# Performance work log

Measured on AMD Instinct MI355X. Metric: run time of the kernel, lower is better.

## Reference

```python
import math
import jax, jax.numpy as jnp
import numpy as np

B, N, D = 16, 4096, 256
N_CAT, N_TPC, N_VPT, N_SP = 16, 8, 4, 16
N_TYPE = N_CAT * N_TPC          # 128
N_VAR = N_TYPE * N_VPT          # 512
THRESH = 0.1
MASK_VAL = jnp.finfo(jnp.float32).min / 2


def _linear(x, w, b):
    # torch nn.Linear: y = x @ W^T + b, W: (out, in)
    return x @ w.T + b


def _level(codes, proj_w, proj_b, K, X, mask, tau):
    """One codebook level: attention of codes over tokens.
    codes: (M, d). Returns H:(B,M,d), w_raw:(B,M)."""
    Q = _linear(codes, proj_w, proj_b)                       # (M, d)
    attn = jnp.einsum('md,bnd->bmn', Q, K) / math.sqrt(D)    # (B, M, N)
    attn = jnp.where(mask[:, None, :], attn, MASK_VAL)
    attn = jnp.clip(attn, -50.0, 50.0)
    G = jnp.nan_to_num(jax.nn.softmax(attn, axis=-1))        # (B, M, N)
    H = jnp.einsum('bmn,bnd->bmd', G, X)                     # (B, M, d)
    w_raw = jnp.linalg.norm(H, axis=-1) / tau                # (B, M)
    return H, w_raw


def _sparsify(w, thr):
    ws = jnp.where(w > thr, w, 0.0)
    return ws / (ws.sum(axis=-1, keepdims=True) + 1e-8)


def _forward(X, positions, category_codes, type_codes, variant_codes,
             spatial_codes, log_tau, cat_w, cat_b, type_w, type_b,
             var_w, var_b, sp_w, sp_b, k_w, k_b, g1_w, g1_b, g2_w, g2_b,
             out_w, out_b, ln_g, ln_b, level_weights, mask):
    tau = jnp.clip(jnp.exp(log_tau[0]) + 0.1, 0.1, 2.0)
    K = _linear(X, k_w, k_b)                                 # (B, N, d)

    # Level 0: category
    H_cat, w_cat_raw = _level(category_codes, cat_w, cat_b, K, X, mask, tau)
    w_cat = jax.nn.softmax(w_cat_raw, axis=-1)
    w_cat_sp = _sparsify(w_cat, THRESH)

    # Level 1: type, gated by category selection
    H_type, w_type_raw = _level(type_codes.reshape(-1, D), type_w, type_b,
                                K, X, mask, tau)
    w_t = (w_type_raw.reshape(-1, N_CAT, N_TPC) * w_cat_sp[:, :, None]
           ).reshape(-1, N_TYPE)
    w_type = jax.nn.softmax(w_t, axis=-1)
    w_type_sp = _sparsify(w_type, THRESH / 2)

    # Level 2: variant, gated by type selection
    H_var, w_var_raw = _level(variant_codes.reshape(-1, D), var_w, var_b,
                              K, X, mask, tau)
    w_type_exp = jnp.repeat(w_type_sp, N_VPT, axis=-1)       # (B, 512)
    w_var = jax.nn.softmax(w_var_raw * w_type_exp, axis=-1)
    w_var_sp = _sparsify(w_var, THRESH / 4)

    # Spatial level (independent)
    H_sp, w_sp_raw = _level(spatial_codes, sp_w, sp_b, K, X, mask, tau)
    w_sp = jax.nn.softmax(w_sp_raw, axis=-1)
    w_sp_sp = _sparsify(w_sp, THRESH)

    z_cat = jnp.einsum('bm,bmd->bd', w_cat_sp, H_cat)
    z_type = jnp.einsum('bm,bmd->bd', w_type_sp, H_type)
    z_var = jnp.einsum('bm,bmd->bd', w_var_sp, H_var)
    z_spatial = jnp.einsum('bm,bmd->bd', w_sp_sp, H_sp)

    # Position gating of category summary
    mask_f = mask.astype(X.dtype)[:, :, None]
    pos_pooled = (positions * mask_f).sum(1) / jnp.maximum(mask_f.sum(1), 1.0)
    gate_in = jnp.concatenate([z_cat, pos_pooled], axis=-1)  # (B, 2d)
    h = jax.nn.gelu(_linear(gate_in, g1_w, g1_b), approximate=False)
    pos_gate = jax.nn.sigmoid(_linear(h, g2_w, g2_b))
    z_cat = z_cat * pos_gate

    # Learned level combine + gated output projection
    lw = jax.nn.softmax(level_weights)
    z = (lw[0] * z_cat + lw[1] * z_type + lw[2] * z_var + lw[3] * z_spatial)
    z = _linear(z, out_w, out_b)
    mu = z.mean(-1, keepdims=True)
    var = z.var(-1, keepdims=True)
    z = (z - mu) / jnp.sqrt(var + 1e-5) * ln_g + ln_b
    return z


def setup_inputs() -> dict:
    key = jax.random.key(0)
    ks = jax.random.split(key, 32)
    s = 1.0 / math.sqrt(D)
    inp = {
        'X': jax.random.normal(ks[0], (B, N, D), jnp.float32),
        'positions': jax.random.normal(ks[1], (B, N, D), jnp.float32),
        'category_codes': jax.random.normal(ks[2], (N_CAT, D)) * 0.02,
        'type_codes': jax.random.normal(ks[3], (N_CAT, N_TPC, D)) * 0.02,
        'variant_codes': jax.random.normal(ks[4], (N_CAT, N_TPC, N_VPT, D)) * 0.02,
        'spatial_codes': jax.random.normal(ks[5], (N_SP, D)) * 0.02,
        'log_tau': jnp.zeros((1,), jnp.float32),
        'cat_w': jax.random.normal(ks[6], (D, D)) * s,
        'cat_b': jnp.zeros((D,)),
        'type_w': jax.random.normal(ks[7], (D, D)) * s,
        'type_b': jnp.zeros((D,)),
        'var_w': jax.random.normal(ks[8], (D, D)) * s,
        'var_b': jnp.zeros((D,)),
        'sp_w': jax.random.normal(ks[9], (D, D)) * s,
        'sp_b': jnp.zeros((D,)),
        'k_w': jax.random.normal(ks[10], (D, D)) * s,
        'k_b': jnp.zeros((D,)),
        'g1_w': jax.random.normal(ks[11], (D, 2 * D)) * s,
        'g1_b': jnp.zeros((D,)),
        'g2_w': jax.random.normal(ks[12], (D, D)) * s,
        'g2_b': jnp.zeros((D,)),
        'out_w': jax.random.normal(ks[13], (D, D)) * s,
        'out_b': jnp.zeros((D,)),
        'ln_g': jnp.ones((D,)),
        'ln_b': jnp.zeros((D,)),
        'level_weights': jnp.ones((4,)) / 4.0,
        'mask': jnp.ones((B, N), jnp.bool_),
    }
    return inp


def reference(X, positions, category_codes, type_codes, variant_codes,
              spatial_codes, log_tau, cat_w, cat_b, type_w, type_b,
              var_w, var_b, sp_w, sp_b, k_w, k_b, g1_w, g1_b, g2_w, g2_b,
              out_w, out_b, ln_g, ln_b, level_weights, mask):
    return _forward(X, positions, category_codes, type_codes, variant_codes,
                    spatial_codes, log_tau, cat_w, cat_b, type_w, type_b,
                    var_w, var_b, sp_w, sp_b, k_w, k_b, g1_w, g1_b,
                    g2_w, g2_b, out_w, out_b, ln_g, ln_b, level_weights, mask)
```

## Files before the change

kernel.cpp:

```cpp
#include <hip/hip_runtime.h>


#define DEV static __device__ __forceinline__

typedef short bf16x8 __attribute__((ext_vector_type(8)));
typedef float f32x4 __attribute__((ext_vector_type(4)));
typedef unsigned short u16x8 __attribute__((ext_vector_type(8)));

DEV float bf2f(unsigned short u) {
  return __uint_as_float(((unsigned int)u) << 16);
}
DEV unsigned short f2bf(float f) {
  unsigned int x = __float_as_uint(f);
  unsigned int r = (x + 0x7fffu + ((x >> 16) & 1u)) >> 16;
  return (unsigned short)r;
}

DEV void gl2lds16(const void* g, void* l) {
  __builtin_amdgcn_global_load_lds(
      (const __attribute__((address_space(1))) unsigned int*)g,
      (__attribute__((address_space(3))) unsigned int*)l, 16, 0, 0);
}

DEV bf16x8 pack8(const float4 a, const float4 b) {
  bf16x8 r;
  r[0] = (short)f2bf(a.x); r[1] = (short)f2bf(a.y);
  r[2] = (short)f2bf(a.z); r[3] = (short)f2bf(a.w);
  r[4] = (short)f2bf(b.x); r[5] = (short)f2bf(b.y);
  r[6] = (short)f2bf(b.z); r[7] = (short)f2bf(b.w);
  return r;
}

DEV size_t pk_off(int rt, int ks) { return ((size_t)rt * 8 + ks) * 512; }

__global__ __launch_bounds__(256) void kproj_mfma(
    const float* __restrict__ X, const float* __restrict__ W,
    const float* __restrict__ bias, unsigned short* __restrict__ Kp) {
  __shared__ __align__(16) unsigned short As[128 * 72];
  __shared__ __align__(16) unsigned short Bs[128 * 72];
  const int m0 = blockIdx.x * 128, c0 = blockIdx.y * 128;
  const int t = threadIdx.x, l = t & 63, w = t >> 6;
  const int wm = (w & 1) * 64, wn = (w >> 1) * 64;
  const f32x4 zero = {0.f, 0.f, 0.f, 0.f};
  f32x4 acc[4][4];
#pragma unroll
  for (int i = 0; i < 4; ++i)
#pragma unroll
    for (int j = 0; j < 4; ++j) acc[i][j] = zero;
  const int rr = t >> 3, cc = (t & 7) * 8;
  for (int kc = 0; kc < 256; kc += 64) {
    __syncthreads();
#pragma unroll
    for (int p = 0; p < 4; ++p) {
      const int r = p * 32 + rr;
      const float* xs = &X[(size_t)(m0 + r) * 256 + kc + cc];
      const float4 a0 = *(const float4*)&xs[0];
      const float4 a1 = *(const float4*)&xs[4];
      *(bf16x8*)&As[r * 72 + cc] = pack8(a0, a1);
      const float* wsrc = &W[(size_t)(c0 + r) * 256 + kc + cc];
      const float4 b0 = *(const float4*)&wsrc[0];
      const float4 b1 = *(const float4*)&wsrc[4];
      *(bf16x8*)&Bs[r * 72 + cc] = pack8(b0, b1);
    }
    __syncthreads();
#pragma unroll
    for (int ks = 0; ks < 2; ++ks) {
      const int koff = ks * 32 + ((l >> 4) & 3) * 8;
      bf16x8 a[4], b[4];
#pragma unroll
      for (int f = 0; f < 4; ++f)
        a[f] = *(const bf16x8*)&As[(wm + f * 16 + (l & 15)) * 72 + koff];
#pragma unroll
      for (int f = 0; f < 4; ++f)
        b[f] = *(const bf16x8*)&Bs[(wn + f * 16 + (l & 15)) * 72 + koff];
#pragma unroll
      for (int i = 0; i < 4; ++i)
#pragma unroll
        for (int j = 0; j < 4; ++j)
          acc[i][j] =
              __builtin_amdgcn_mfma_f32_16x16x32_bf16(a[i], b[j], acc[i][j],
                                                      0, 0, 0);
    }
  }
  const int q = (l >> 4) & 3;
#pragma unroll
  for (int j = 0; j < 4; ++j) {
    const int c = c0 + wn + j * 16 + (l & 15);
    const float bv = bias[c];
#pragma unroll
    for (int i = 0; i < 4; ++i) {
      const int mrow = m0 + wm + i * 16 + q * 4;
#pragma unroll
      for (int r = 0; r < 4; ++r) {
        const int m = mrow + r;
        Kp[pk_off(m >> 4, c >> 5) + ((m & 15) + 16 * ((c >> 3) & 3)) * 8 +
           (c & 7)] = f2bf(acc[i][j][r] + bv);
      }
    }
  }
}

__global__ __launch_bounds__(256) void xT_kern(const float* __restrict__ X,
                                               unsigned short* __restrict__ XTp) {
  __shared__ float Ls[64][65];
  const int tn = blockIdx.x, td = blockIdx.y, b = blockIdx.z;
  const int t = threadIdx.x;
  const int nl = t >> 2, dp = (t & 3) * 16;
  const float* src =
      X + ((size_t)b * 4096 + tn * 64 + nl) * 256 + td * 64 + dp;
#pragma unroll
  for (int v = 0; v < 4; ++v) {
    const float4 x = *(const float4*)&src[v * 4];
    Ls[nl][dp + v * 4 + 0] = x.x;
    Ls[nl][dp + v * 4 + 1] = x.y;
    Ls[nl][dp + v * 4 + 2] = x.z;
    Ls[nl][dp + v * 4 + 3] = x.w;
  }
  __syncthreads();
  const int dl = t >> 2, np = (t & 3) * 16;
  u16x8 h0, h1;
#pragma unroll
  for (int j = 0; j < 8; ++j) h0[j] = f2bf(Ls[np + j][dl]);
#pragma unroll
  for (int j = 0; j < 8; ++j) h1[j] = f2bf(Ls[np + 8 + j][dl]);
  const int d = td * 64 + dl;
  const int n0g = tn * 64 + np;
  const int n1g = n0g + 8;
  unsigned short* dst = XTp + (size_t)b * 1048576;
  const size_t o0 = (((size_t)(d >> 4) * 128) + (n0g >> 5)) * 512 +
                    ((d & 15) + 16 * ((n0g >> 3) & 3)) * 8;
  const size_t o1 = (((size_t)(d >> 4) * 128) + (n1g >> 5)) * 512 +
                    ((d & 15) + 16 * ((n1g >> 3) & 3)) * 8;
  *(u16x8*)&dst[o0] = h0;
  *(u16x8*)&dst[o1] = h1;
}

__global__ __launch_bounds__(256) void qproj_kern(
    const float* __restrict__ cat_codes, const float* __restrict__ type_codes,
    const float* __restrict__ var_codes, const float* __restrict__ sp_codes,
    const float* __restrict__ cat_w, const float* __restrict__ cat_b,
    const float* __restrict__ type_w, const float* __restrict__ type_b,
    const float* __restrict__ var_w, const float* __restrict__ var_b,
    const float* __restrict__ sp_w, const float* __restrict__ sp_b,
    unsigned short* __restrict__ Qp) {
  const int m = blockIdx.x;
  const int t = threadIdx.x;
  const size_t off = pk_off(m >> 4, t >> 5) +
                     ((m & 15) + 16 * ((t >> 3) & 3)) * 8 + (t & 7);
  if (m >= 672) {
    Qp[off] = 0;
    return;
  }
  const float* code;
  const float* W;
  const float* bias;
  if (m < 16)       { code = cat_codes  + m * 256;         W = cat_w;  bias = cat_b; }
  else if (m < 144) { code = type_codes + (m - 16) * 256;  W = type_w; bias = type_b; }
  else if (m < 656) { code = var_codes  + (m - 144) * 256; W = var_w;  bias = var_b; }
  else              { code = sp_codes   + (m - 656) * 256; W = sp_w;   bias = sp_b; }
  __shared__ float xs[256];
  xs[t] = code[t];
  __syncthreads();
  float a = bias[t];
  const float* wr = W + (size_t)t * 256;
  for (int k = 0; k < 256; k += 4) {
    const float4 w = *(const float4*)&wr[k];
    a = fmaf(w.x, xs[k], a);
    a = fmaf(w.y, xs[k + 1], a);
    a = fmaf(w.z, xs[k + 2], a);
    a = fmaf(w.w, xs[k + 3], a);
  }
  Qp[off] = f2bf(a);
}

__global__ __launch_bounds__(256, 3) void attn_fused(
    const unsigned short* __restrict__ Qp, const unsigned short* __restrict__ Kp,
    const unsigned short* __restrict__ XTp,
    const unsigned char* __restrict__ mask, float* __restrict__ H,
    float* __restrict__ lsum) {
  __shared__ __align__(16) unsigned short Ks[16384];
  __shared__ __align__(16) unsigned short Plds[64 * 72];
  __shared__ unsigned char msk[1024];
  const int combo = blockIdx.x;
  const int m0 = blockIdx.y * 64;
  const int b = combo >> 2;
  const int nbase = (combo & 3) * 1024;
  const int t = threadIdx.x, l = t & 63, w = t >> 6;
  const int l15 = l & 15, q = l >> 4;
  ((uchar4*)msk)[t] = ((const uchar4*)(mask + (size_t)b * 4096 + nbase))[t];
  const int mt_g = (m0 >> 4) + w;
  bf16x8 qf[8];
#pragma unroll
  for (int ks = 0; ks < 8; ++ks)
    qf[ks] = *(const bf16x8*)&Qp[pk_off(mt_g, ks) + l * 8];
  const f32x4 zero = {0.f, 0.f, 0.f, 0.f};
  f32x4 accO[4][4];
#pragma unroll
  for (int i = 0; i < 4; ++i)
#pragma unroll
    for (int j = 0; j < 4; ++j) accO[i][j] = zero;
  f32x4 rs = zero;
  const unsigned short* XTb = XTp + (size_t)b * 1048576;
  const unsigned short* Kchunk0 = Kp + ((size_t)b * 256 + (nbase >> 4)) * 4096;
#pragma unroll
  for (int i = 0; i < 8; ++i)
    gl2lds16(Kchunk0 + (w * 8 + i) * 512 + l * 8, &Ks[(w * 8 + i) * 512]);
  for (int c = 0; c < 16; ++c) {
    __syncthreads();
    const int nst0 = (nbase >> 5) + c * 2;
    bf16x8 xf[2][4];
#pragma unroll
    for (int ks2 = 0; ks2 < 2; ++ks2)
#pragma unroll
      for (int dj = 0; dj < 4; ++dj)
        xf[ks2][dj] = *(const bf16x8*)&XTb[((size_t)(4 * w + dj) * 128 +
                                            nst0 + ks2) * 512 + l * 8];
    f32x4 accS[4];
#pragma unroll
    for (int f = 0; f < 4; ++f) accS[f] = zero;
    __builtin_amdgcn_s_setprio(1);
#pragma unroll
    for (int ks = 0; ks < 8; ++ks) {
      bf16x8 kf[4];
#pragma unroll
      for (int f = 0; f < 4; ++f)
        kf[f] = *(const bf16x8*)&Ks[(f * 8 + ks) * 512 + l * 8];
#pragma unroll
      for (int f = 0; f < 4; ++f)
        accS[f] = __builtin_amdgcn_mfma_f32_16x16x32_bf16(qf[ks], kf[f],
                                                          accS[f], 0, 0, 0);
    }
    __builtin_amdgcn_s_setprio(0);
#pragma unroll
    for (int f = 0; f < 4; ++f) {
      const bool mk = msk[c * 64 + f * 16 + l15] != 0;
#pragma unroll
      for (int r = 0; r < 4; ++r) {
        float s = accS[f][r] * 0.0625f;
        s = fminf(fmaxf(s, -50.f), 50.f);
        if (!mk) s = -50.f;
        const float e = __expf(s);
        Plds[(w * 16 + q * 4 + r) * 72 + f * 16 + l15] = f2bf(e);
        rs[r] += e;
      }
    }
    __syncthreads();
    if (c < 15) {
      const unsigned short* src = Kchunk0 + (size_t)(c + 1) * 16384;
#pragma unroll
      for (int i = 0; i < 8; ++i)
        gl2lds16(src + (w * 8 + i) * 512 + l * 8, &Ks[(w * 8 + i) * 512]);
    }
#pragma unroll
    for (int ks2 = 0; ks2 < 2; ++ks2) {
      bf16x8 pf[4];
#pragma unroll
      for (int mt = 0; mt < 4; ++mt)
        pf[mt] = *(const bf16x8*)&Plds[(mt * 16 + l15) * 72 + ks2 * 32 + q * 8];
      __builtin_amdgcn_s_setprio(1);
#pragma unroll
      for (int mt = 0; mt < 4; ++mt)
#pragma unroll
        for (int dj = 0; dj < 4; ++dj)
          accO[mt][dj] = __builtin_amdgcn_mfma_f32_16x16x32_bf16(
              pf[mt], xf[ks2][dj], accO[mt][dj], 0, 0, 0);
      __builtin_amdgcn_s_setprio(0);
    }
  }
#pragma unroll
  for (int r = 0; r < 4; ++r) {
    float v = rs[r];
    v += __shfl_xor(v, 1, 64);
    v += __shfl_xor(v, 2, 64);
    v += __shfl_xor(v, 4, 64);
    v += __shfl_xor(v, 8, 64);
    const int m = m0 + w * 16 + q * 4 + r;
    if (l15 == 0 && m < 672) atomicAdd(&lsum[b * 672 + m], v);
  }
#pragma unroll
  for (int mt = 0; mt < 4; ++mt) {
    const int mbase = m0 + mt * 16 + q * 4;
#pragma unroll
    for (int dj = 0; dj < 4; ++dj) {
      const int d = w * 64 + dj * 16 + l15;
#pragma unroll
      for (int r = 0; r < 4; ++r) {
        const int m = mbase + r;
        if (m < 672)
          atomicAdd(&H[((size_t)b * 672 + m) * 256 + d], accO[mt][dj][r]);
      }
    }
  }
}

__global__ __launch_bounds__(256) void hfinal_ip(
    float* __restrict__ H, const float* __restrict__ lsum,
    const float* __restrict__ log_tau, float* __restrict__ wraw) {
  const int bm = blockIdx.x;
  const int t = threadIdx.x;
  __shared__ float red[256];
  const float inv = 1.0f / lsum[bm];
  const float v = H[(size_t)bm * 256 + t] * inv;
  H[(size_t)bm * 256 + t] = v;
  red[t] = v * v;
  __syncthreads();
  for (int s = 128; s > 0; s >>= 1) {
    if (t < s) red[t] += red[t + s];
    __syncthreads();
  }
  if (t == 0) {
    const float tau = fminf(fmaxf(expf(log_tau[0]) + 0.1f, 0.1f), 2.0f);
    wraw[bm] = sqrtf(red[0]) / tau;
  }
}

__global__ __launch_bounds__(256) void pospool_kern(
    const float* __restrict__ pos, const unsigned char* __restrict__ mask,
    float* __restrict__ pacc, float* __restrict__ cnt) {
  const int b = blockIdx.x, seg = blockIdx.y, t = threadIdx.x;
  const int dg = t & 63;
  const int nl = t >> 6;
  const int n0 = seg * 128;
  float4 acc = make_float4(0.f, 0.f, 0.f, 0.f);
  float c = 0.f;
  const float* pb = pos + (size_t)b * 4096 * 256;
  for (int j = 0; j < 32; ++j) {
    const int n = n0 + j * 4 + nl;
    const unsigned char mk = mask[(size_t)b * 4096 + n];
    if (mk) {
      const float4 v = *(const float4*)&pb[(size_t)n * 256 + dg * 4];
      acc.x += v.x; acc.y += v.y; acc.z += v.z; acc.w += v.w;
      if (dg == 0) c += 1.f;
    }
  }
  __shared__ float4 red4[256];
  __shared__ float redc[4];
  red4[t] = acc;
  if (dg == 0) redc[nl] = c;
  __syncthreads();
  if (t < 64) {
    float4 s = red4[t];
    const float4 s1 = red4[t + 64], s2 = red4[t + 128], s3 = red4[t + 192];
    s.x += s1.x + s2.x + s3.x;
    s.y += s1.y + s2.y + s3.y;
    s.z += s1.z + s2.z + s3.z;
    s.w += s1.w + s2.w + s3.w;
    float* pa = pacc + b * 256 + t * 4;
    atomicAdd(pa + 0, s.x);
    atomicAdd(pa + 1, s.y);
    atomicAdd(pa + 2, s.z);
    atomicAdd(pa + 3, s.w);
    if (t == 0) atomicAdd(&cnt[b], redc[0] + redc[1] + redc[2] + redc[3]);
  }
}

DEV float wave_max(float v) {
#pragma unroll
  for (int m = 1; m < 64; m <<= 1) v = fmaxf(v, __shfl_xor(v, m, 64));
  return v;
}
DEV float wave_sum(float v) {
#pragma unroll
  for (int m = 1; m < 64; m <<= 1) v += __shfl_xor(v, m, 64);
  return v;
}

__global__ __launch_bounds__(256) void combine_kern(
    const float* __restrict__ wraw, const float* __restrict__ H,
    float* __restrict__ zbuf) {
  const int b = blockIdx.x, t = threadIdx.x, l = t & 63;
  __shared__ float wr[672];
  __shared__ float wsp[672];
  for (int i = t; i < 672; i += 256) wr[i] = wraw[b * 672 + i];
  __syncthreads();
  {
    const float v = (l < 16) ? wr[l] : -1e30f;
    const float mx = wave_max(v);
    const float e = (l < 16) ? expf(wr[l] - mx) : 0.f;
    const float s = wave_sum(e);
    float w = e / s;
    w = (w > 0.1f) ? w : 0.f;
    const float s2 = wave_sum(w);
    if (l < 16) wsp[l] = w / (s2 + 1e-8f);
  }
  __syncthreads();
  {
    const float L0 = wr[16 + l] * wsp[l >> 3];
    const float L1 = wr[16 + 64 + l] * wsp[(64 + l) >> 3];
    const float mx = wave_max(fmaxf(L0, L1));
    const float e0 = expf(L0 - mx), e1 = expf(L1 - mx);
    const float s = wave_sum(e0 + e1);
    float w0 = e0 / s, w1 = e1 / s;
    w0 = (w0 > 0.05f) ? w0 : 0.f;
    w1 = (w1 > 0.05f) ? w1 : 0.f;
    const float s2 = wave_sum(w0 + w1);
    const float inv2 = 1.f / (s2 + 1e-8f);
    wsp[16 + l] = w0 * inv2;
    wsp[16 + 64 + l] = w1 * inv2;
  }
  __syncthreads();
  {
    float Lv[8];
    float lm = -1e30f;
#pragma unroll
    for (int j = 0; j < 8; ++j) {
      const int i = l * 8 + j;
      Lv[j] = wr[144 + i] * wsp[16 + (i >> 2)];
      lm = fmaxf(lm, Lv[j]);
    }
    const float mx = wave_max(lm);
    float ls = 0.f;
#pragma unroll
    for (int j = 0; j < 8; ++j) {
      Lv[j] = expf(Lv[j] - mx);
      ls += Lv[j];
    }
    const float s = wave_sum(ls);
    const float inv = 1.f / s;
    float ls2 = 0.f;
#pragma unroll
    for (int j = 0; j < 8; ++j) {
      float w = Lv[j] * inv;
      w = (w > 0.025f) ? w : 0.f;
      Lv[j] = w;
      ls2 += w;
    }
    const float s2 = wave_sum(ls2);
    const float inv2 = 1.f / (s2 + 1e-8f);
#pragma unroll
    for (int j = 0; j < 8; ++j) wsp[144 + l * 8 + j] = Lv[j] * inv2;
  }
  __syncthreads();
  {
    const float v = (l < 16) ? wr[656 + l] : -1e30f;
    const float mx = wave_max(v);
    const float e = (l < 16) ? expf(wr[656 + l] - mx) : 0.f;
    const float s = wave_sum(e);
    float w = e / s;
    w = (w > 0.1f) ? w : 0.f;
    const float s2 = wave_sum(w);
    if (l < 16) wsp[656 + l] = w / (s2 + 1e-8f);
  }
  __syncthreads();
  const float* Hb = H + (size_t)b * 672 * 256 + t;
  float z0 = 0.f, z1 = 0.f, z2 = 0.f, z3 = 0.f;
  for (int m = 0; m < 16; ++m) {
    const float wv = wsp[m];
    if (wv != 0.f) z0 = fmaf(wv, Hb[(size_t)m * 256], z0);
  }
  for (int m = 0; m < 128; ++m) {
    const float wv = wsp[16 + m];
    if (wv != 0.f) z1 = fmaf(wv, Hb[(size_t)(16 + m) * 256], z1);
  }
  for (int m = 0; m < 512; ++m) {
    const float wv = wsp[144 + m];
    if (wv != 0.f) z2 = fmaf(wv, Hb[(size_t)(144 + m) * 256], z2);
  }
  for (int m = 0; m < 16; ++m) {
    const float wv = wsp[656 + m];
    if (wv != 0.f) z3 = fmaf(wv, Hb[(size_t)(656 + m) * 256], z3);
  }
  zbuf[(b * 4 + 0) * 256 + t] = z0;
  zbuf[(b * 4 + 1) * 256 + t] = z1;
  zbuf[(b * 4 + 2) * 256 + t] = z2;
  zbuf[(b * 4 + 3) * 256 + t] = z3;
}

__global__ __launch_bounds__(256) void gate_kern(
    const float* __restrict__ zbuf, const float* __restrict__ pacc,
    const float* __restrict__ cnt, const float* __restrict__ g1_w,
    const float* __restrict__ g1_b, const float* __restrict__ g2_w,
    const float* __restrict__ g2_b, const float* __restrict__ out_w,
    const float* __restrict__ out_b, const float* __restrict__ ln_g,
    const float* __restrict__ ln_b, const float* __restrict__ lvlw,
    float* __restrict__ out) {
  const int b = blockIdx.x, t = threadIdx.x;
  __shared__ float gin[512];
  __shared__ float hb[256];
  __shared__ float zc[256];
  __shared__ float red[256];
  const float z0 = zbuf[(b * 4 + 0) * 256 + t];
  gin[t] = z0;
  const float c = fmaxf(cnt[b], 1.0f);
  gin[256 + t] = pacc[b * 256 + t] / c;
  __syncthreads();
  float a = g1_b[t];
  const float* w1 = g1_w + (size_t)t * 512;
  for (int k = 0; k < 512; k += 4) {
    const float4 w = *(const float4*)&w1[k];
    a = fmaf(w.x, gin[k], a);
    a = fmaf(w.y, gin[k + 1], a);
    a = fmaf(w.z, gin[k + 2], a);
    a = fmaf(w.w, gin[k + 3], a);
  }
  const float hg = 0.5f * a * (1.0f + erff(a * 0.7071067811865475f));
  hb[t] = hg;
  __syncthreads();
  float a2 = g2_b[t];
  const float* w2 = g2_w + (size_t)t * 256;
  for (int k = 0; k < 256; k += 4) {
    const float4 w = *(const float4*)&w2[k];
    a2 = fmaf(w.x, hb[k], a2);
    a2 = fmaf(w.y, hb[k + 1], a2);
    a2 = fmaf(w.z, hb[k + 2], a2);
    a2 = fmaf(w.w, hb[k + 3], a2);
  }
  const float pg = 1.0f / (1.0f + expf(-a2));
  const float l0 = lvlw[0], l1 = lvlw[1], l2 = lvlw[2], l3 = lvlw[3];
  const float mx = fmaxf(fmaxf(l0, l1), fmaxf(l2, l3));
  const float e0 = expf(l0 - mx), e1 = expf(l1 - mx);
  const float e2 = expf(l2 - mx), e3 = expf(l3 - mx);
  const float einv = 1.0f / (e0 + e1 + e2 + e3);
  const float zmix = (e0 * z0 * pg + e1 * zbuf[(b * 4 + 1) * 256 + t] +
                      e2 * zbuf[(b * 4 + 2) * 256 + t] +
                      e3 * zbuf[(b * 4 + 3) * 256 + t]) * einv;
  zc[t] = zmix;
  __syncthreads();
  float o = out_b[t];
  const float* wo = out_w + (size_t)t * 256;
  for (int k = 0; k < 256; k += 4) {
    const float4 w = *(const float4*)&wo[k];
    o = fmaf(w.x, zc[k], o);
    o = fmaf(w.y, zc[k + 1], o);
    o = fmaf(w.z, zc[k + 2], o);
    o = fmaf(w.w, zc[k + 3], o);
  }
  red[t] = o;
  __syncthreads();
  for (int s = 128; s > 0; s >>= 1) {
    if (t < s) red[t] += red[t + s];
    __syncthreads();
  }
  const float mu = red[0] / 256.f;
  __syncthreads();
  red[t] = o * o;
  __syncthreads();
  for (int s = 128; s > 0; s >>= 1) {
    if (t < s) red[t] += red[t + s];
    __syncthreads();
  }
  const float var = red[0] / 256.f - mu * mu;
  out[b * 256 + t] = (o - mu) * rsqrtf(var + 1e-5f) * ln_g[t] + ln_b[t];
}

extern "C" void kernel_launch(void* const* d_in, const int* in_sizes, int n_in,
                              void* d_out, int out_size, void* d_ws,
                              size_t ws_size, hipStream_t stream) {
  (void)in_sizes; (void)n_in; (void)out_size; (void)ws_size;
  const float* X          = (const float*)d_in[0];
  const float* positions  = (const float*)d_in[1];
  const float* cat_codes  = (const float*)d_in[2];
  const float* type_codes = (const float*)d_in[3];
  const float* var_codes  = (const float*)d_in[4];
  const float* sp_codes   = (const float*)d_in[5];
  const float* log_tau    = (const float*)d_in[6];
  const float* cat_w      = (const float*)d_in[7];
  const float* cat_b      = (const float*)d_in[8];
  const float* type_w     = (const float*)d_in[9];
  const float* type_b     = (const float*)d_in[10];
  const float* var_w      = (const float*)d_in[11];
  const float* var_b      = (const float*)d_in[12];
  const float* sp_w       = (const float*)d_in[13];
  const float* sp_b       = (const float*)d_in[14];
  const float* k_w        = (const float*)d_in[15];
  const float* k_b        = (const float*)d_in[16];
  const float* g1_w       = (const float*)d_in[17];
  const float* g1_b       = (const float*)d_in[18];
  const float* g2_w       = (const float*)d_in[19];
  const float* g2_b       = (const float*)d_in[20];
  const float* out_w      = (const float*)d_in[21];
  const float* out_b      = (const float*)d_in[22];
  const float* ln_g       = (const float*)d_in[23];
  const float* ln_b       = (const float*)d_in[24];
  const float* lvlw       = (const float*)d_in[25];
  const unsigned char* mask = (const unsigned char*)d_in[26];

  char* ws = (char*)d_ws;
  constexpr size_t O_KP  = 0;
  constexpr size_t O_XT  = 33554432;
  constexpr size_t O_QP  = 67108864;
  constexpr size_t O_H   = 67469312;
  constexpr size_t O_L   = 78479360;
  constexpr size_t O_WR  = 78522368;
  constexpr size_t O_PA  = 78565376;
  constexpr size_t O_CNT = 78581760;
  constexpr size_t O_Z   = 78581824;

  unsigned short* Kp  = (unsigned short*)(ws + O_KP);
  unsigned short* XTp = (unsigned short*)(ws + O_XT);
  unsigned short* Qp  = (unsigned short*)(ws + O_QP);
  float* H            = (float*)(ws + O_H);
  float* lsum         = (float*)(ws + O_L);
  float* wraw         = (float*)(ws + O_WR);
  float* pacc         = (float*)(ws + O_PA);
  float* cnt          = (float*)(ws + O_CNT);
  float* zbuf         = (float*)(ws + O_Z);
  float* out          = (float*)d_out;

  hipMemsetAsync(lsum, 0, 16 * 672 * 4, stream);
  hipMemsetAsync(H, 0, 11010048, stream);
  hipMemsetAsync(pacc, 0, 16 * 256 * 4, stream);
  hipMemsetAsync(cnt, 0, 64, stream);

  qproj_kern<<<dim3(704), 256, 0, stream>>>(
      cat_codes, type_codes, var_codes, sp_codes, cat_w, cat_b, type_w, type_b,
      var_w, var_b, sp_w, sp_b, Qp);
  kproj_mfma<<<dim3(512, 2), 256, 0, stream>>>(X, k_w, k_b, Kp);
  xT_kern<<<dim3(64, 4, 16), 256, 0, stream>>>(X, XTp);
  pospool_kern<<<dim3(16, 32), 256, 0, stream>>>(positions, mask, pacc, cnt);

  attn_fused<<<dim3(64, 11), 256, 0, stream>>>(Qp, Kp, XTp, mask, H, lsum);

  hfinal_ip<<<dim3(16 * 672), 256, 0, stream>>>(H, lsum, log_tau, wraw);
  combine_kern<<<dim3(16), 256, 0, stream>>>(wraw, H, zbuf);
  gate_kern<<<dim3(16), 256, 0, stream>>>(zbuf, pacc, cnt, g1_w, g1_b, g2_w,
                                          g2_b, out_w, out_b, ln_g, ln_b, lvlw,
                                          out);
}
```

Baseline: 455.6 us.

## Read K fragments directly from global, double-buffer P, remap grid for XCD locality

The attention kernel no longer stages K chunks into LDS with async global-to-LDS copies. Each wave now loads its K fragments straight from global memory, and the P tile is double-buffered so only one barrier per chunk is needed. The grid becomes 1D and is remapped so that blocks sharing a batch and n-slice land on the same XCD, aiming for better L2 reuse of K and X. LDS use and sync overhead drop, but each wave issues redundant global loads of K that now rely on the cache rather than shared memory.

```diff
diff --git a/kernel.cpp b/kernel.cpp
--- a/kernel.cpp
+++ b/kernel.cpp
@@ -14,12 +14,6 @@
   unsigned int x = __float_as_uint(f);
   unsigned int r = (x + 0x7fffu + ((x >> 16) & 1u)) >> 16;
   return (unsigned short)r;
-}
-
-DEV void gl2lds16(const void* g, void* l) {
-  __builtin_amdgcn_global_load_lds(
-      (const __attribute__((address_space(1))) unsigned int*)g,
-      (__attribute__((address_space(3))) unsigned int*)l, 16, 0, 0);
 }
 
 DEV bf16x8 pack8(const float4 a, const float4 b) {
@@ -178,13 +172,16 @@
     const unsigned short* __restrict__ XTp,
     const unsigned char* __restrict__ mask, float* __restrict__ H,
     float* __restrict__ lsum) {
-  __shared__ __align__(16) unsigned short Ks[16384];
-  __shared__ __align__(16) unsigned short Plds[64 * 72];
+  __shared__ __align__(16) unsigned short Plds[2][64 * 72];
   __shared__ unsigned char msk[1024];
-  const int combo = blockIdx.x;
-  const int m0 = blockIdx.y * 64;
-  const int b = combo >> 2;
-  const int nbase = (combo & 3) * 1024;
+  const int g = blockIdx.x;
+  const int xcd = g & 7;
+  const int slot = g >> 3;
+  const int nsl = slot & 3;
+  const int gid = xcd * 22 + (slot >> 2);
+  const int b = gid / 11;
+  const int m0 = (gid % 11) * 64;
+  const int nbase = nsl * 1024;
   const int t = threadIdx.x, l = t & 63, w = t >> 6;
   const int l15 = l & 15, q = l >> 4;
   ((uchar4*)msk)[t] = ((const uchar4*)(mask + (size_t)b * 4096 + nbase))[t];
@@ -201,12 +198,10 @@
     for (int j = 0; j < 4; ++j) accO[i][j] = zero;
   f32x4 rs = zero;
   const unsigned short* XTb = XTp + (size_t)b * 1048576;
-  const unsigned short* Kchunk0 = Kp + ((size_t)b * 256 + (nbase >> 4)) * 4096;
-#pragma unroll
-  for (int i = 0; i < 8; ++i)
-    gl2lds16(Kchunk0 + (w * 8 + i) * 512 + l * 8, &Ks[(w * 8 + i) * 512]);
+  const unsigned short* Kc = Kp + ((size_t)b * 256 + (nbase >> 4)) * 4096;
+  __syncthreads();
   for (int c = 0; c < 16; ++c) {
-    __syncthreads();
+    const int cur = c & 1;
     const int nst0 = (nbase >> 5) + c * 2;
     bf16x8 xf[2][4];
 #pragma unroll
@@ -215,6 +210,7 @@
       for (int dj = 0; dj < 4; ++dj)
         xf[ks2][dj] = *(const bf16x8*)&XTb[((size_t)(4 * w + dj) * 128 +
                                             nst0 + ks2) * 512 + l * 8];
+    const unsigned short* Kch = Kc + (size_t)c * 16384;
     f32x4 accS[4];
 #pragma unroll
     for (int f = 0; f < 4; ++f) accS[f] = zero;
@@ -224,7 +220,7 @@
       bf16x8 kf[4];
 #pragma unroll
       for (int f = 0; f < 4; ++f)
-        kf[f] = *(const bf16x8*)&Ks[(f * 8 + ks) * 512 + l * 8];
+        kf[f] = *(const bf16x8*)&Kch[(f * 8 + ks) * 512 + l * 8];
 #pragma unroll
       for (int f = 0; f < 4; ++f)
         accS[f] = __builtin_amdgcn_mfma_f32_16x16x32_bf16(qf[ks], kf[f],
@@ -240,23 +236,18 @@
         s = fminf(fmaxf(s, -50.f), 50.f);
         if (!mk) s = -50.f;
         const float e = __expf(s);
-        Plds[(w * 16 + q * 4 + r) * 72 + f * 16 + l15] = f2bf(e);
+        Plds[cur][(w * 16 + q * 4 + r) * 72 + f * 16 + l15] = f2bf(e);
         rs[r] += e;
       }
     }
     __syncthreads();
-    if (c < 15) {
-      const unsigned short* src = Kchunk0 + (size_t)(c + 1) * 16384;
-#pragma unroll
-      for (int i = 0; i < 8; ++i)
-        gl2lds16(src + (w * 8 + i) * 512 + l * 8, &Ks[(w * 8 + i) * 512]);
-    }
 #pragma unroll
     for (int ks2 = 0; ks2 < 2; ++ks2) {
       bf16x8 pf[4];
 #pragma unroll
       for (int mt = 0; mt < 4; ++mt)
-        pf[mt] = *(const bf16x8*)&Plds[(mt * 16 + l15) * 72 + ks2 * 32 + q * 8];
+        pf[mt] =
+            *(const bf16x8*)&Plds[cur][(mt * 16 + l15) * 72 + ks2 * 32 + q * 8];
       __builtin_amdgcn_s_setprio(1);
 #pragma unroll
       for (int mt = 0; mt < 4; ++mt)
@@ -609,7 +600,7 @@
   xT_kern<<<dim3(64, 4, 16), 256, 0, stream>>>(X, XTp);
   pospool_kern<<<dim3(16, 32), 256, 0, stream>>>(positions, mask, pacc, cnt);
 
-  attn_fused<<<dim3(64, 11), 256, 0, stream>>>(Qp, Kp, XTp, mask, H, lsum);
+  attn_fused<<<dim3(704), 256, 0, stream>>>(Qp, Kp, XTp, mask, H, lsum);
 
   hfinal_ip<<<dim3(16 * 672), 256, 0, stream>>>(H, lsum, log_tau, wraw);
   combine_kern<<<dim3(16), 256, 0, stream>>>(wraw, H, zbuf);
```

Result: slower. 553.2 us (+21.4%).
